# Optimization experiments

Measured on AMD Instinct MI355X. Metric: run time of the kernel, lower is better.

## Reference

```python
import jax, jax.numpy as jnp
import numpy as np

EPS = 1e-12  # torch F.normalize eps

def _cam(fmap, w):
    # torch: sum over C of w[1,C,R,1,1] * fmap[B,C,1,H,W] -> (B,R,H,W)
    # expressed as an efficient contraction (1x1 conv / GEMM)
    return jnp.einsum('bchw,rc->brhw', fmap, w)

def _embedding(fmap, w, b):
    pooled = fmap.mean(axis=(-2, -1))           # (B,C) AdaptiveAvgPool2d(1)
    return pooled @ w.T + b                      # (B,R)

def _certainty(cam):
    B, R = cam.shape[:2]
    flat = cam.reshape(B, R, -1)
    return jnp.std(flat, axis=-1, ddof=1)        # torch .std() is unbiased

def _avgpool_to(x, out_hw):
    # adaptive avg pool with integer ratio == reshape-mean
    B, R, H, W = x.shape
    oh, ow = out_hw
    return x.reshape(B, R, oh, H // oh, ow, W // ow).mean(axis=(3, 5))

def _link(low_cam, high_cam):
    low_cam = jax.lax.stop_gradient(low_cam)
    high_cam = jax.lax.stop_gradient(high_cam)
    if low_cam.shape[2:] != high_cam.shape[2:]:
        low_cam = _avgpool_to(low_cam, high_cam.shape[2:])
    B = low_cam.shape[0]
    lo = low_cam.reshape(B, low_cam.shape[1], -1)
    hi = high_cam.reshape(B, high_cam.shape[1], -1)
    lo = lo / jnp.maximum(jnp.linalg.norm(lo, axis=-1, keepdims=True), EPS)
    hi = hi / jnp.maximum(jnp.linalg.norm(hi, axis=-1, keepdims=True), EPS)
    return jnp.einsum('bmi,bni->mn', lo, hi) / B

def setup_inputs() -> dict:
    key = jax.random.key(0)
    ks = jax.random.split(key, 6)
    B, R = 64, 128
    chans = [512, 1024, 2048]
    hws = [28, 14, 7]
    inp = {}
    for l in range(3):
        inp[f'fmap{l}'] = jax.random.normal(ks[l], (B, chans[l], hws[l], hws[l]), dtype=jnp.float32)
        inp[f'w{l}'] = jax.random.normal(ks[3 + l], (R, chans[l]), dtype=jnp.float32) * 0.02
        inp[f'b{l}'] = jnp.zeros((R,), dtype=jnp.float32)
    return inp

def reference(fmap0, fmap1, fmap2, w0, b0, w1, b1, w2, b2):
    fmaps = [fmap0, fmap1, fmap2]
    ws = [w0, w1, w2]
    bs = [b0, b1, b2]
    embeddings = [_embedding(f, w, b) for f, w, b in zip(fmaps, ws, bs)]
    cams = [_cam(f, w) for f, w in zip(fmaps, ws)]
    certainties = [_certainty(c) for c in cams]
    links = [_link(cams[l - 1], cams[l]) for l in range(1, 3)]
    return (*embeddings, *certainties, *links)
```

## Files before the change

### kernel.cpp

```cpp
#include <hip/hip_runtime.h>
#include <stdint.h>

#define R 128
#define NB 64

#define CAM1_OFF  0
#define CAM2_OFF  1605632
#define POOL0_OFF 2007040
#define POOL1_OFF 3612672
#define WB_OFF    4014080
#define ACCS_OFF  4243456
#define ACCQ_OFF  4268032
#define PSQ_OFF   4292608
#define INVHI_OFF 4308992
#define INVLO_OFF 4325376

typedef __bf16 bf16;
typedef bf16 v2bf __attribute__((ext_vector_type(2)));
typedef bf16 v8bf __attribute__((ext_vector_type(8)));
typedef float f4v __attribute__((ext_vector_type(4)));

#define ASM_BARRIER() asm volatile("s_waitcnt lgkmcnt(0)\n\ts_barrier" ::: "memory")

__global__ void prep_w(const float* __restrict__ w0, const float* __restrict__ w1,
                       const float* __restrict__ w2, bf16* __restrict__ wb,
                       float* __restrict__ ws, float* __restrict__ out) {
    int id = blockIdx.x * 256 + threadIdx.x;
    if (id < 65536) ws[ACCS_OFF + id] = 0.f;
    if (id < 32768) out[49152 + id] = 0.f;
    float v;
    if (id < 65536)       v = w0[id];
    else if (id < 196608) v = w1[id - 65536];
    else                  v = w2[id - 196608];
    wb[id] = (bf16)v;
}

__global__ __launch_bounds__(512) void cam_gemm(
    const float* __restrict__ f0, const float* __restrict__ f1,
    const float* __restrict__ f2, const bf16* __restrict__ wb,
    float* __restrict__ ws) {
    __shared__ __align__(16) char ldsRaw[55296];
#define LBUFB(u) ((bf16*)(ldsRaw + (u) * 9216))
#define LBUFA(u) ((bf16*)(ldsRaw + 18432 + (u) * 18432))

    int bid = blockIdx.x, tid = threadIdx.x;
    int lvl, b, i0, VW;
    if (bid < 64)       { lvl = 2; b = bid; i0 = 0; VW = 49; }
    else if (bid < 320) { int t = bid - 64; lvl = 1; b = t >> 2;
                          int ti = t & 3; i0 = ti * 56; VW = ti < 3 ? 56 : 28; }
    else                { int t = bid - 320; lvl = 0; b = t / 14;
                          int ti = t - b * 14; i0 = ti * 56; VW = 56; }
    const int C  = (lvl == 0) ? 512 : (lvl == 1) ? 1024 : 2048;
    const int HW = (lvl == 0) ? 784 : (lvl == 1) ? 196  : 49;
    const float* fmap = (lvl == 0) ? f0 : (lvl == 1) ? f1 : f2;
    const bf16*  wbl  = wb + ((lvl == 0) ? 0 : (lvl == 1) ? 65536 : 196608);

    int d = tid >> 4;
    int ku2 = d * 2;
    int i4 = (tid & 15) * 4;
    int i4eff = min(i4, VW - 4);
    int gbase = b * C * HW + ku2 * HW + i0 + i4eff;
    int ldsd[4];
    int i4c[4];
#pragma unroll
    for (int e = 0; e < 4; ++e) {
        int i = i4 + e;
        int grp = (d >> 2) ^ ((i >> 3) & 7);
        ldsd[e] = i * 72 + grp * 8 + (d & 3) * 2;
        i4c[e] = min(i, 48);
    }
    int am = tid >> 2;
    int akb = (tid & 3) * 16;
    const bf16* awsrc = wbl + am * C + akb;
    int axor = (am >> 3) & 7;
    int ac0 = (tid & 3) * 2;
    int aldsd0 = am * 72 + ((ac0    ) ^ axor) * 8;
    int aldsd1 = am * 72 + ((ac0 + 1) ^ axor) * 8;

    const int lane = tid & 63, wave = tid >> 6;
    const int lm = lane & 15, q = lane >> 4;
    const int wm = (wave >> 1) * 32, wn = (wave & 1) * 32;
    int irow[2], ixor[2];
#pragma unroll
    for (int sn = 0; sn < 2; ++sn) {
        irow[sn] = wn + sn * 16 + lm;
        ixor[sn] = (irow[sn] >> 3) & 7;
    }
    int arowl[2], axorl[2];
#pragma unroll
    for (int sm = 0; sm < 2; ++sm) {
        arowl[sm] = wm + sm * 16 + lm;
        axorl[sm] = (arowl[sm] >> 3) & 7;
    }

    auto loadT = [&](int kc, float4 (&r)[2]) {
        if (lvl != 2) {
            const float* p = fmap + gbase + kc * HW;
            r[0] = *(const float4*)p;
            r[1] = *(const float4*)(p + HW);
        } else {
            const float* p = fmap + b * C * 49 + (kc + ku2) * 49;
            r[0].x = p[i4c[0]]; r[0].y = p[i4c[1]];
            r[0].z = p[i4c[2]]; r[0].w = p[i4c[3]];
            r[1].x = p[49 + i4c[0]]; r[1].y = p[49 + i4c[1]];
            r[1].z = p[49 + i4c[2]]; r[1].w = p[49 + i4c[3]];
        }
    };
    auto loadW = [&](int kc, v8bf (&w)[2]) {
        w[0] = *(const v8bf*)(awsrc + kc);
        w[1] = *(const v8bf*)(awsrc + kc + 8);
    };
    auto stage = [&](float4 (&r)[2], v8bf (&w)[2], bf16* bufB, bf16* bufA) {
        v2bf t0 = { (bf16)r[0].x, (bf16)r[1].x };
        v2bf t1 = { (bf16)r[0].y, (bf16)r[1].y };
        v2bf t2 = { (bf16)r[0].z, (bf16)r[1].z };
        v2bf t3 = { (bf16)r[0].w, (bf16)r[1].w };
        *(v2bf*)&bufB[ldsd[0]] = t0;
        *(v2bf*)&bufB[ldsd[1]] = t1;
        *(v2bf*)&bufB[ldsd[2]] = t2;
        *(v2bf*)&bufB[ldsd[3]] = t3;
        *(v8bf*)&bufA[aldsd0] = w[0];
        *(v8bf*)&bufA[aldsd1] = w[1];
    };

    f4v acc[2][2] = {};
    auto comp = [&](const bf16* bufB, const bf16* bufA) {
#pragma unroll
        for (int ks = 0; ks < 64; ks += 32) {
            int cq = (ks >> 3) + q;
            v8bf af[2];
#pragma unroll
            for (int sm = 0; sm < 2; ++sm)
                af[sm] = *(const v8bf*)&bufA[arowl[sm] * 72 + (cq ^ axorl[sm]) * 8];
            v8bf bfr[2];
#pragma unroll
            for (int sn = 0; sn < 2; ++sn)
                bfr[sn] = *(const v8bf*)&bufB[irow[sn] * 72 + (cq ^ ixor[sn]) * 8];
#pragma unroll
            for (int sm = 0; sm < 2; ++sm)
#pragma unroll
                for (int sn = 0; sn < 2; ++sn)
                    acc[sm][sn] = __builtin_amdgcn_mfma_f32_16x16x32_bf16(
                        af[sm], bfr[sn], acc[sm][sn], 0, 0, 0);
        }
    };

    const int nIter = C >> 6;
    float4 rT[4][2];
    v8bf   rW[4][2];
    loadT(0, rT[0]);   loadW(0, rW[0]);
    loadT(64, rT[1]);  loadW(64, rW[1]);
    loadT(128, rT[2]); loadW(128, rW[2]);
    loadT(192, rT[3]); loadW(192, rW[3]);
    for (int t = 0; t < nIter; t += 4) {
#pragma unroll
        for (int u = 0; u < 4; ++u) {
            stage(rT[u], rW[u], LBUFB(u & 1), LBUFA(u & 1));
            ASM_BARRIER();
            if (t + u + 4 < nIter) { loadT((t + u + 4) << 6, rT[u]);
                                     loadW((t + u + 4) << 6, rW[u]); }
            comp(LBUFB(u & 1), LBUFA(u & 1));
        }
    }

    __syncthreads();
    float* tile = (float*)ldsRaw;
#pragma unroll
    for (int sn = 0; sn < 2; ++sn)
#pragma unroll
        for (int sm = 0; sm < 2; ++sm)
#pragma unroll
            for (int reg = 0; reg < 4; ++reg)
                tile[(wm + sm * 16 + q * 4 + reg) * 68 + wn + sn * 16 + lm] =
                    acc[sm][sn][reg];
    __syncthreads();

    int row = tid >> 2, seg = tid & 3;
    long grow = (long)b * 128 + row;
    const float* trow = tile + row * 68;
    float* camrow = (lvl == 1) ? ws + CAM1_OFF + grow * 196 + i0
                  : (lvl == 2) ? ws + CAM2_OFF + grow * 49 : (float*)0;
    float s = 0.f, qq = 0.f;
    const f4v* tr4 = (const f4v*)(trow + seg * 16);
#pragma unroll
    for (int g = 0; g < 4; ++g) {
        f4v v4 = tr4[g];
#pragma unroll
        for (int e = 0; e < 4; ++e) {
            int col = seg * 16 + g * 4 + e;
            if (col < VW) {
                float v = v4[e];
                s += v; qq += v * v;
                if (lvl) camrow[col] = v;
            }
        }
    }
    s += __shfl_xor(s, 1);  s += __shfl_xor(s, 2);
    qq += __shfl_xor(qq, 1); qq += __shfl_xor(qq, 2);
    if (seg == 0) {
        atomicAdd(&ws[ACCS_OFF + lvl * 8192 + grow], s);
        atomicAdd(&ws[ACCQ_OFF + lvl * 8192 + grow], qq);
    }
    if (lvl == 0) {
        float ps = 0.f;
        float* prow = ws + POOL0_OFF + grow * 196 + (i0 / 56) * 14;
        for (int j = seg; j < 14; j += 4) {
            float v = 0.25f * (trow[2 * j] + trow[2 * j + 1] +
                               trow[28 + 2 * j] + trow[28 + 2 * j + 1]);
            prow[j] = v; ps += v * v;
        }
        ps += __shfl_xor(ps, 1); ps += __shfl_xor(ps, 2);
        if (seg == 0) atomicAdd(&ws[PSQ_OFF + grow], ps);
    } else if (lvl == 1) {
        float ps = 0.f;
        int tt = i0 / 56;
        int npj = (VW == 56) ? 14 : 7;
        for (int pj = seg; pj < npj; pj += 4) {
            int sub = pj / 7, jj = pj - sub * 7;
            const float* tr2 = trow + sub * 28;
            float v = 0.25f * (tr2[2 * jj] + tr2[2 * jj + 1] +
                               tr2[14 + 2 * jj] + tr2[14 + 2 * jj + 1]);
            ws[POOL1_OFF + grow * 49 + (2 * tt + sub) * 7 + jj] = v;
            ps += v * v;
        }
        ps += __shfl_xor(ps, 1); ps += __shfl_xor(ps, 2);
        if (seg == 0) atomicAdd(&ws[PSQ_OFF + 8192 + grow], ps);
    }
#undef LBUFB
#undef LBUFA
}

__global__ __launch_bounds__(256) void finalize_k(
    float* __restrict__ ws, const float* __restrict__ b0,
    const float* __restrict__ b1, const float* __restrict__ b2,
    float* __restrict__ out) {
    int id = blockIdx.x * 256 + threadIdx.x;
    if (id < 16384) {
        float qn = ws[PSQ_OFF + id];
        ws[INVLO_OFF + id] = (1.0f / 64.0f) / fmaxf(sqrtf(qn), 1e-12f);
    }
    int lvl = id >> 13, row = id & 8191;
    float HWf = (lvl == 0) ? 784.f : (lvl == 1) ? 196.f : 49.f;
    float s = ws[ACCS_OFF + id], qq = ws[ACCQ_OFF + id];
    float mean = s / HWf;
    const float* bias = (lvl == 0) ? b0 : (lvl == 1) ? b1 : b2;
    out[id] = mean + bias[row & 127];
    float var = fmaxf(qq - s * mean, 0.f) / (HWf - 1.f);
    out[24576 + id] = sqrtf(var);
    if (lvl >= 1)
        ws[INVHI_OFF + (lvl - 1) * 8192 + row] = 1.0f / fmaxf(sqrtf(qq), 1e-12f);
}

__device__ inline v8bf load_frag8(const float* __restrict__ row, int k0, int K) {
    v8bf f;
    if (k0 + 8 <= K && (K & 3) == 0) {
        float4 a = *(const float4*)(row + k0);
        float4 c = *(const float4*)(row + k0 + 4);
        f[0] = (bf16)a.x; f[1] = (bf16)a.y; f[2] = (bf16)a.z; f[3] = (bf16)a.w;
        f[4] = (bf16)c.x; f[5] = (bf16)c.y; f[6] = (bf16)c.z; f[7] = (bf16)c.w;
    } else {
#pragma unroll
        for (int j = 0; j < 8; ++j)
            f[j] = (k0 + j < K) ? (bf16)row[k0 + j] : (bf16)0.f;
    }
    return f;
}

__global__ __launch_bounds__(256) void link_mfma_k(const float* __restrict__ ws,
                                                   float* __restrict__ out) {
    int bid = blockIdx.x, tid = threadIdx.x;
    int lk = bid >> 7, rem = bid & 127;
    int b = rem >> 1, mh = rem & 1;
    const int K = lk ? 49 : 196;
    const float* lo = ws + (lk ? POOL1_OFF : POOL0_OFF) + (long)(b * 128 + mh * 64) * K;
    const float* hi = ws + (lk ? CAM2_OFF : CAM1_OFF) + (long)b * 128 * K;
    const float* ihi = ws + INVHI_OFF + lk * 8192 + b * 128;
    const float* ilo = ws + INVLO_OFF + lk * 8192 + b * 128 + mh * 64;
    int lane = tid & 63, wv = tid >> 6;
    int lm = lane & 15, q = lane >> 4;
    int wm = (wv >> 1) * 32, wn = (wv & 1) * 64;
    f4v acc[2][4] = {};
    for (int kc = 0; kc < K; kc += 32) {
        v8bf af[2], bff[4];
#pragma unroll
        for (int sm = 0; sm < 2; ++sm)
            af[sm] = load_frag8(lo + (long)(wm + sm * 16 + lm) * K, kc + q * 8, K);
#pragma unroll
        for (int sn = 0; sn < 4; ++sn)
            bff[sn] = load_frag8(hi + (long)(wn + sn * 16 + lm) * K, kc + q * 8, K);
#pragma unroll
        for (int sm = 0; sm < 2; ++sm)
#pragma unroll
            for (int sn = 0; sn < 4; ++sn)
                acc[sm][sn] = __builtin_amdgcn_mfma_f32_16x16x32_bf16(
                    af[sm], bff[sn], acc[sm][sn], 0, 0, 0);
    }
    float fl[2][4];
#pragma unroll
    for (int sm = 0; sm < 2; ++sm)
#pragma unroll
        for (int reg = 0; reg < 4; ++reg)
            fl[sm][reg] = ilo[wm + sm * 16 + q * 4 + reg];
    float* ob = out + 49152 + lk * 16384;
#pragma unroll
    for (int sn = 0; sn < 4; ++sn) {
        int n = wn + sn * 16 + lm;
        float sh = ihi[n];
#pragma unroll
        for (int sm = 0; sm < 2; ++sm) {
#pragma unroll
            for (int reg = 0; reg < 4; ++reg) {
                int m = mh * 64 + wm + sm * 16 + q * 4 + reg;
                atomicAdd(&ob[m * 128 + n], acc[sm][sn][reg] * sh * fl[sm][reg]);
            }
        }
    }
}

extern "C" void kernel_launch(void* const* d_in, const int* in_sizes, int n_in,
                              void* d_out, int out_size, void* d_ws, size_t ws_size,
                              hipStream_t stream) {
    const float* f0 = (const float*)d_in[0];
    const float* w0 = (const float*)d_in[1];
    const float* b0 = (const float*)d_in[2];
    const float* f1 = (const float*)d_in[3];
    const float* w1 = (const float*)d_in[4];
    const float* b1 = (const float*)d_in[5];
    const float* f2 = (const float*)d_in[6];
    const float* w2 = (const float*)d_in[7];
    const float* b2 = (const float*)d_in[8];
    float* ws = (float*)d_ws;
    float* out = (float*)d_out;
    bf16* wb = (bf16*)(ws + WB_OFF);

    prep_w<<<1792, 256, 0, stream>>>(w0, w1, w2, wb, ws, out);
    cam_gemm<<<1216, 512, 0, stream>>>(f0, f1, f2, wb, ws);
    finalize_k<<<96, 256, 0, stream>>>(ws, b0, b1, b2, out);
    link_mfma_k<<<256, 256, 0, stream>>>(ws, out);
}
```

Baseline: 284.5 us.

## Split-K the deep-channel CAM GEMM blocks and move stats and pooling to post kernel

Levels 1 and 2 now split the channel reduction into 512-wide chunks across more blocks, so per-block work is even and the grid is larger (1664 blocks instead of 1216). Partial CAM tiles are combined with float atomics into a workspace that prep_w now zeroes. Sum, sum-of-squares and 2x2 pooling for levels 1 and 2 move out of the GEMM epilogue into a new wave-per-row post kernel. The cost is extra atomic traffic, a larger zeroing pass and an extra read of the CAM buffers, plus summation order that is no longer deterministic.

```diff
diff --git a/kernel.cpp b/kernel.cpp
--- a/kernel.cpp
+++ b/kernel.cpp
@@ -26,13 +26,16 @@
                        const float* __restrict__ w2, bf16* __restrict__ wb,
                        float* __restrict__ ws, float* __restrict__ out) {
     int id = blockIdx.x * 256 + threadIdx.x;
+    ws[id] = 0.f;
     if (id < 65536) ws[ACCS_OFF + id] = 0.f;
     if (id < 32768) out[49152 + id] = 0.f;
-    float v;
-    if (id < 65536)       v = w0[id];
-    else if (id < 196608) v = w1[id - 65536];
-    else                  v = w2[id - 196608];
-    wb[id] = (bf16)v;
+    if (id < 458752) {
+        float v;
+        if (id < 65536)       v = w0[id];
+        else if (id < 196608) v = w1[id - 65536];
+        else                  v = w2[id - 196608];
+        wb[id] = (bf16)v;
+    }
 }
 
 __global__ __launch_bounds__(512) void cam_gemm(
@@ -44,12 +47,14 @@
 #define LBUFA(u) ((bf16*)(ldsRaw + 18432 + (u) * 18432))
 
     int bid = blockIdx.x, tid = threadIdx.x;
-    int lvl, b, i0, VW;
-    if (bid < 64)       { lvl = 2; b = bid; i0 = 0; VW = 49; }
-    else if (bid < 320) { int t = bid - 64; lvl = 1; b = t >> 2;
-                          int ti = t & 3; i0 = ti * 56; VW = ti < 3 ? 56 : 28; }
-    else                { int t = bid - 320; lvl = 0; b = t / 14;
-                          int ti = t - b * 14; i0 = ti * 56; VW = 56; }
+    int lvl, b, i0, VW, kb;
+    if (bid < 256)      { lvl = 2; b = bid >> 2; kb = (bid & 3) * 512;
+                          i0 = 0; VW = 49; }
+    else if (bid < 768) { int t = bid - 256; lvl = 1; b = t >> 3; int r = t & 7;
+                          int ti = r >> 1; kb = (r & 1) * 512;
+                          i0 = ti * 56; VW = ti < 3 ? 56 : 28; }
+    else                { int t = bid - 768; lvl = 0; b = t / 14;
+                          int ti = t - b * 14; kb = 0; i0 = ti * 56; VW = 56; }
     const int C  = (lvl == 0) ? 512 : (lvl == 1) ? 1024 : 2048;
     const int HW = (lvl == 0) ? 784 : (lvl == 1) ? 196  : 49;
     const float* fmap = (lvl == 0) ? f0 : (lvl == 1) ? f1 : f2;
@@ -59,7 +64,7 @@
     int ku2 = d * 2;
     int i4 = (tid & 15) * 4;
     int i4eff = min(i4, VW - 4);
-    int gbase = b * C * HW + ku2 * HW + i0 + i4eff;
+    int gbase = b * C * HW + (kb + ku2) * HW + i0 + i4eff;
     int ldsd[4];
     int i4c[4];
 #pragma unroll
@@ -71,7 +76,7 @@
     }
     int am = tid >> 2;
     int akb = (tid & 3) * 16;
-    const bf16* awsrc = wbl + am * C + akb;
+    const bf16* awsrc = wbl + am * C + kb + akb;
     int axor = (am >> 3) & 7;
     int ac0 = (tid & 3) * 2;
     int aldsd0 = am * 72 + ((ac0    ) ^ axor) * 8;
@@ -99,7 +104,7 @@
             r[0] = *(const float4*)p;
             r[1] = *(const float4*)(p + HW);
         } else {
-            const float* p = fmap + b * C * 49 + (kc + ku2) * 49;
+            const float* p = fmap + b * C * 49 + (kb + kc + ku2) * 49;
             r[0].x = p[i4c[0]]; r[0].y = p[i4c[1]];
             r[0].z = p[i4c[2]]; r[0].w = p[i4c[3]];
             r[1].x = p[49 + i4c[0]]; r[1].y = p[49 + i4c[1]];
@@ -145,20 +150,19 @@
         }
     };
 
-    const int nIter = C >> 6;
     float4 rT[4][2];
     v8bf   rW[4][2];
     loadT(0, rT[0]);   loadW(0, rW[0]);
     loadT(64, rT[1]);  loadW(64, rW[1]);
     loadT(128, rT[2]); loadW(128, rW[2]);
     loadT(192, rT[3]); loadW(192, rW[3]);
-    for (int t = 0; t < nIter; t += 4) {
+    for (int t = 0; t < 8; t += 4) {
 #pragma unroll
         for (int u = 0; u < 4; ++u) {
             stage(rT[u], rW[u], LBUFB(u & 1), LBUFA(u & 1));
             ASM_BARRIER();
-            if (t + u + 4 < nIter) { loadT((t + u + 4) << 6, rT[u]);
-                                     loadW((t + u + 4) << 6, rW[u]); }
+            if (t + u + 4 < 8) { loadT((t + u + 4) << 6, rT[u]);
+                                 loadW((t + u + 4) << 6, rW[u]); }
             comp(LBUFB(u & 1), LBUFA(u & 1));
         }
     }
@@ -178,30 +182,24 @@
     int row = tid >> 2, seg = tid & 3;
     long grow = (long)b * 128 + row;
     const float* trow = tile + row * 68;
-    float* camrow = (lvl == 1) ? ws + CAM1_OFF + grow * 196 + i0
-                  : (lvl == 2) ? ws + CAM2_OFF + grow * 49 : (float*)0;
-    float s = 0.f, qq = 0.f;
-    const f4v* tr4 = (const f4v*)(trow + seg * 16);
-#pragma unroll
-    for (int g = 0; g < 4; ++g) {
-        f4v v4 = tr4[g];
-#pragma unroll
-        for (int e = 0; e < 4; ++e) {
-            int col = seg * 16 + g * 4 + e;
-            if (col < VW) {
-                float v = v4[e];
-                s += v; qq += v * v;
-                if (lvl) camrow[col] = v;
+    if (lvl == 0) {
+        float s = 0.f, qq = 0.f;
+        const f4v* tr4 = (const f4v*)(trow + seg * 16);
+#pragma unroll
+        for (int g = 0; g < 4; ++g) {
+            f4v v4 = tr4[g];
+#pragma unroll
+            for (int e = 0; e < 4; ++e) {
+                int col = seg * 16 + g * 4 + e;
+                if (col < 56) { float v = v4[e]; s += v; qq += v * v; }
             }
         }
-    }
-    s += __shfl_xor(s, 1);  s += __shfl_xor(s, 2);
-    qq += __shfl_xor(qq, 1); qq += __shfl_xor(qq, 2);
-    if (seg == 0) {
-        atomicAdd(&ws[ACCS_OFF + lvl * 8192 + grow], s);
-        atomicAdd(&ws[ACCQ_OFF + lvl * 8192 + grow], qq);
-    }
-    if (lvl == 0) {
+        s += __shfl_xor(s, 1);  s += __shfl_xor(s, 2);
+        qq += __shfl_xor(qq, 1); qq += __shfl_xor(qq, 2);
+        if (seg == 0) {
+            atomicAdd(&ws[ACCS_OFF + grow], s);
+            atomicAdd(&ws[ACCQ_OFF + grow], qq);
+        }
         float ps = 0.f;
         float* prow = ws + POOL0_OFF + grow * 196 + (i0 / 56) * 14;
         for (int j = seg; j < 14; j += 4) {
@@ -211,44 +209,75 @@
         }
         ps += __shfl_xor(ps, 1); ps += __shfl_xor(ps, 2);
         if (seg == 0) atomicAdd(&ws[PSQ_OFF + grow], ps);
-    } else if (lvl == 1) {
-        float ps = 0.f;
-        int tt = i0 / 56;
-        int npj = (VW == 56) ? 14 : 7;
-        for (int pj = seg; pj < npj; pj += 4) {
-            int sub = pj / 7, jj = pj - sub * 7;
-            const float* tr2 = trow + sub * 28;
-            float v = 0.25f * (tr2[2 * jj] + tr2[2 * jj + 1] +
-                               tr2[14 + 2 * jj] + tr2[14 + 2 * jj + 1]);
-            ws[POOL1_OFF + grow * 49 + (2 * tt + sub) * 7 + jj] = v;
-            ps += v * v;
-        }
-        ps += __shfl_xor(ps, 1); ps += __shfl_xor(ps, 2);
-        if (seg == 0) atomicAdd(&ws[PSQ_OFF + 8192 + grow], ps);
+    } else {
+        float* camrow = (lvl == 1) ? ws + CAM1_OFF + grow * 196 + i0
+                                   : ws + CAM2_OFF + grow * 49;
+        const f4v* tr4 = (const f4v*)(trow + seg * 16);
+#pragma unroll
+        for (int g = 0; g < 4; ++g) {
+            f4v v4 = tr4[g];
+#pragma unroll
+            for (int e = 0; e < 4; ++e) {
+                int col = seg * 16 + g * 4 + e;
+                if (col < VW) atomicAdd(&camrow[col], v4[e]);
+            }
+        }
     }
 #undef LBUFB
 #undef LBUFA
 }
 
-__global__ __launch_bounds__(256) void finalize_k(
+__global__ __launch_bounds__(256) void post_k(
     float* __restrict__ ws, const float* __restrict__ b0,
     const float* __restrict__ b1, const float* __restrict__ b2,
     float* __restrict__ out) {
-    int id = blockIdx.x * 256 + threadIdx.x;
-    if (id < 16384) {
-        float qn = ws[PSQ_OFF + id];
-        ws[INVLO_OFF + id] = (1.0f / 64.0f) / fmaxf(sqrtf(qn), 1e-12f);
-    }
-    int lvl = id >> 13, row = id & 8191;
-    float HWf = (lvl == 0) ? 784.f : (lvl == 1) ? 196.f : 49.f;
-    float s = ws[ACCS_OFF + id], qq = ws[ACCQ_OFF + id];
-    float mean = s / HWf;
-    const float* bias = (lvl == 0) ? b0 : (lvl == 1) ? b1 : b2;
-    out[id] = mean + bias[row & 127];
-    float var = fmaxf(qq - s * mean, 0.f) / (HWf - 1.f);
-    out[24576 + id] = sqrtf(var);
-    if (lvl >= 1)
+    __shared__ float plds[4 * 196];
+    int gw = blockIdx.x * 4 + (threadIdx.x >> 6);
+    int lane = threadIdx.x & 63;
+    int lvl = gw >> 13, row = gw & 8191;
+    if (lvl == 0) {
+        if (lane == 0) {
+            float s = ws[ACCS_OFF + row], qq = ws[ACCQ_OFF + row];
+            float mean = s / 784.f;
+            out[row] = mean + b0[row & 127];
+            out[24576 + row] = sqrtf(fmaxf(qq - s * mean, 0.f) / 783.f);
+            float qn = ws[PSQ_OFF + row];
+            ws[INVLO_OFF + row] = (1.0f / 64.0f) / fmaxf(sqrtf(qn), 1e-12f);
+        }
+        return;
+    }
+    const int HW = (lvl == 1) ? 196 : 49;
+    const float* cam = ws + ((lvl == 1) ? CAM1_OFF : CAM2_OFF) + (long)row * HW;
+    float* myl = plds + (threadIdx.x >> 6) * 196;
+    float s = 0.f, qq = 0.f;
+    for (int j = lane; j < HW; j += 64) {
+        float v = cam[j]; s += v; qq += v * v;
+        if (lvl == 1) myl[j] = v;
+    }
+#pragma unroll
+    for (int o = 32; o; o >>= 1) { s += __shfl_xor(s, o); qq += __shfl_xor(qq, o); }
+    if (lane == 0) {
+        float HWf = (float)HW;
+        float mean = s / HWf;
+        const float* bias = (lvl == 1) ? b1 : b2;
+        out[lvl * 8192 + row] = mean + bias[row & 127];
+        out[24576 + lvl * 8192 + row] = sqrtf(fmaxf(qq - s * mean, 0.f) / (HWf - 1.f));
         ws[INVHI_OFF + (lvl - 1) * 8192 + row] = 1.0f / fmaxf(sqrtf(qq), 1e-12f);
+    }
+    if (lvl == 1) {
+        float ps = 0.f;
+        if (lane < 49) {
+            int oh = lane / 7, ow = lane - oh * 7;
+            int ii = oh * 28 + ow * 2;
+            float v = 0.25f * (myl[ii] + myl[ii + 1] + myl[ii + 14] + myl[ii + 15]);
+            ws[POOL1_OFF + (long)row * 49 + lane] = v;
+            ps = v * v;
+        }
+#pragma unroll
+        for (int o = 32; o; o >>= 1) ps += __shfl_xor(ps, o);
+        if (lane == 0)
+            ws[INVLO_OFF + 8192 + row] = (1.0f / 64.0f) / fmaxf(sqrtf(ps), 1e-12f);
+    }
 }
 
 __device__ inline v8bf load_frag8(const float* __restrict__ row, int k0, int K) {
@@ -333,8 +362,8 @@
     float* out = (float*)d_out;
     bf16* wb = (bf16*)(ws + WB_OFF);
 
-    prep_w<<<1792, 256, 0, stream>>>(w0, w1, w2, wb, ws, out);
-    cam_gemm<<<1216, 512, 0, stream>>>(f0, f1, f2, wb, ws);
-    finalize_k<<<96, 256, 0, stream>>>(ws, b0, b1, b2, out);
+    prep_w<<<7840, 256, 0, stream>>>(w0, w1, w2, wb, ws, out);
+    cam_gemm<<<1664, 512, 0, stream>>>(f0, f1, f2, wb, ws);
+    post_k<<<6144, 256, 0, stream>>>(ws, b0, b1, b2, out);
     link_mfma_k<<<256, 256, 0, stream>>>(ws, out);
 }
```

Result: slower. 491.5 us (+72.7%).
